# Kernel tuning notes

Measured on AMD Instinct MI355X. Metric: run time of the kernel, lower is better.

Reference implementation:

```python
import jax, jax.numpy as jnp
import numpy as np

IN_CH = 128
OUT_CH = 128
N_NODES = 50000
N_EDGES = 800000
BN_EPS = 1e-5


def setup_inputs() -> dict:
    key = jax.random.key(0)
    k_x, k_e, k_wl, k_bl, k_wr = jax.random.split(key, 5)
    x = jax.random.normal(k_x, (N_NODES, IN_CH), dtype=jnp.float32)
    edge_index = jax.random.randint(k_e, (2, N_EDGES), 0, N_NODES, dtype=jnp.int64)
    s = 1.0 / np.sqrt(IN_CH)
    W_l = jax.random.uniform(k_wl, (OUT_CH, IN_CH), jnp.float32, -s, s)  # lin_l: aggregated neighbors
    b_l = jax.random.uniform(k_bl, (OUT_CH,), jnp.float32, -s, s)
    W_r = jax.random.uniform(k_wr, (OUT_CH, IN_CH), jnp.float32, -s, s)  # lin_r: root/self
    gamma = jnp.ones((OUT_CH,), jnp.float32)
    beta = jnp.zeros((OUT_CH,), jnp.float32)
    return {"x": x, "edge_index": edge_index, "W_l": W_l, "b_l": b_l,
            "W_r": W_r, "gamma": gamma, "beta": beta}


def reference(x, edge_index, W_l, b_l, W_r, gamma, beta):
    n = x.shape[0]
    src, dst = edge_index[0], edge_index[1]
    # gather source features and mean-aggregate at destination nodes
    msgs = x[src]                                              # [E, C_in]
    agg = jax.ops.segment_sum(msgs, dst, num_segments=n)      # [N, C_in]
    deg = jax.ops.segment_sum(jnp.ones((edge_index.shape[1],), x.dtype), dst, num_segments=n)
    mean_agg = agg / jnp.maximum(deg, 1.0)[:, None]
    # SAGEConv: lin_l(aggregated) + lin_r(self)
    h = mean_agg @ W_l.T + b_l + x @ W_r.T                     # [N, C_out]
    # BatchNorm1d (training-mode batch statistics, biased variance)
    mu = h.mean(axis=0)
    var = ((h - mu) ** 2).mean(axis=0)
    h = (h - mu) * jax.lax.rsqrt(var + BN_EPS) * gamma + beta
    return jax.nn.relu(h)
```

## Files before the change

### kernel.cpp

```cpp
#include <hip/hip_runtime.h>

#define CH 128
#define BN_EPS 1e-5f

typedef unsigned int uint32;
typedef unsigned short ushort16;
using f32x2  = __attribute__((ext_vector_type(2))) float;
using f32x4  = __attribute__((ext_vector_type(4))) float;
using bf16x8 = __attribute__((ext_vector_type(8))) short;

__device__ __forceinline__ ushort16 f2b(float f) {
    uint32 u = __float_as_uint(f);
    return (ushort16)((u + 0x7FFFu + ((u >> 16) & 1u)) >> 16);
}
__device__ __forceinline__ uint32 pk2(float a, float b) {
    return (uint32)f2b(a) | ((uint32)f2b(b) << 16);
}
__device__ __forceinline__ float blo(uint32 u) { return __uint_as_float(u << 16); }
__device__ __forceinline__ float bhi(uint32 u) { return __uint_as_float(u & 0xFFFF0000u); }

__global__ __launch_bounds__(256) void sage_prep(
    const float* __restrict__ x, const void* __restrict__ ei,
    const float* __restrict__ Wl, const float* __restrict__ Wr,
    int* __restrict__ head, int2* __restrict__ pair,
    uint32* __restrict__ xb4, uint2* __restrict__ xq8,
    ushort16* __restrict__ wct, float* __restrict__ bn,
    int nEdges, int nNodes, int total8)
{
    const int* pi = (const int*)ei;
    int lane = threadIdx.x & 63;
    int probe = pi[lane * 2 + 1];
    bool is64 = (__ballot(probe != 0) == 0ULL);

    int idx = blockIdx.x * 256 + threadIdx.x;

    const float4* x4 = (const float4*)x;
    float4 a = make_float4(0, 0, 0, 0), b = make_float4(0, 0, 0, 0);
    bool hasC = (idx < total8);
    if (hasC) { a = x4[2 * idx]; b = x4[2 * idx + 1]; }

    if (idx < nEdges) {
        int s, d;
        if (is64) {
            const long long* p = (const long long*)ei;
            s = (int)p[idx];
            d = (int)p[nEdges + idx];
        } else {
            s = pi[idx];
            d = pi[nEdges + idx];
        }
        int old = atomicExch(&head[d], idx);
        pair[idx] = make_int2(old, s);
    }

    if (hasC) {
        uint4 o;
        o.x = pk2(a.x, a.y); o.y = pk2(a.z, a.w);
        o.z = pk2(b.x, b.y); o.w = pk2(b.z, b.w);
        ((uint4*)xb4)[idx] = o;

        int qa = __builtin_amdgcn_cvt_pk_fp8_f32(a.x, a.y, 0, false);
        qa = __builtin_amdgcn_cvt_pk_fp8_f32(a.z, a.w, qa, true);
        int qb = __builtin_amdgcn_cvt_pk_fp8_f32(b.x, b.y, 0, false);
        qb = __builtin_amdgcn_cvt_pk_fp8_f32(b.z, b.w, qb, true);
        xq8[idx] = make_uint2((uint32)qa, (uint32)qb);
    }

    if (blockIdx.x < 128) {
        int widx = blockIdx.x * 256 + threadIdx.x;
        int co = widx >> 8, k = widx & 255;
        float v = (k < 128) ? Wr[co * 128 + k] : Wl[co * 128 + (k - 128)];
        wct[widx] = f2b(v);
    }
    if (blockIdx.x == 0) bn[threadIdx.x] = 0.f;
    if (blockIdx.x == 1 && threadIdx.x < 32)
        ((uint32*)(xq8))[(size_t)total8 * 2 + threadIdx.x] = 0;
}

__global__ __launch_bounds__(256) void sage_init(int* __restrict__ head, int nNodes) {
    int i = blockIdx.x * 256 + threadIdx.x;
    if (i < nNodes) head[i] = -1;
}

__global__ __launch_bounds__(256) void sage_aggregate(
    const char* __restrict__ xq, const int* __restrict__ head,
    const int2* __restrict__ pair, uint32* __restrict__ mean_b, int nNodes)
{
    int wid = blockIdx.x * 4 + (threadIdx.x >> 6);
    int nbase = wid * 8;
    if (nbase >= nNodes) return;
    int lane = threadIdx.x & 63;
    int chain = lane >> 3;
    int sub = lane & 7;

    const int ZROW = nNodes;

    int cur = -1;
    if (lane < 8) {
        int n = nbase + lane;
        cur = (n < nNodes) ? head[n] : -1;
    }
    int cnt = 0;
    f32x2 acc2[8];
    #pragma unroll
    for (int i = 0; i < 8; ++i) acc2[i] = (f32x2){0.f, 0.f};

    int2 pr = make_int2(-1, ZROW);
    if (cur >= 0) pr = pair[cur];

    while (__ballot(cur >= 0) != 0ULL) {
        int nxt = pr.x;
        int2 prn = make_int2(-1, ZROW);
        if (cur >= 0 && nxt >= 0) prn = pair[nxt];

        int s = __shfl(pr.y, chain);
        uint4 u = *(const uint4*)(xq + ((size_t)s << 7) + sub * 16);
        #pragma unroll
        for (int w = 0; w < 4; ++w) {
            uint32 uw = (&u.x)[w];
            acc2[w * 2 + 0] += __builtin_amdgcn_cvt_pk_f32_fp8((int)uw, false);
            acc2[w * 2 + 1] += __builtin_amdgcn_cvt_pk_f32_fp8((int)uw, true);
        }
        if (cur >= 0) { ++cnt; cur = nxt; }
        pr = prn;
    }

    int cn = __shfl(cnt, chain);
    float inv = 1.0f / fmaxf((float)cn, 1.0f);
    int n = nbase + chain;
    if (n < nNodes) {
        uint4 o0 = make_uint4(pk2(acc2[0][0] * inv, acc2[0][1] * inv),
                              pk2(acc2[1][0] * inv, acc2[1][1] * inv),
                              pk2(acc2[2][0] * inv, acc2[2][1] * inv),
                              pk2(acc2[3][0] * inv, acc2[3][1] * inv));
        uint4 o1 = make_uint4(pk2(acc2[4][0] * inv, acc2[4][1] * inv),
                              pk2(acc2[5][0] * inv, acc2[5][1] * inv),
                              pk2(acc2[6][0] * inv, acc2[6][1] * inv),
                              pk2(acc2[7][0] * inv, acc2[7][1] * inv));
        char* base = (char*)mean_b + (size_t)n * 256 + sub * 32;
        *(uint4*)base = o0;
        *(uint4*)(base + 16) = o1;
    }
}

__global__ __launch_bounds__(256) void sage_gemm(
    const ushort16* __restrict__ xb, const ushort16* __restrict__ mean_b,
    const ushort16* __restrict__ wct, const float* __restrict__ bl,
    ushort16* __restrict__ hb, float* __restrict__ bn, int nNodes)
{
    __shared__ ushort16 wsh[8 * 8 * 64 * 8];
    __shared__ float redS[4][CH];
    __shared__ float redQ[4][CH];

    int tid = threadIdx.x;
    int wave = tid >> 6, lane = tid & 63;
    int col = lane & 15, kg = lane >> 4;

    #pragma unroll
    for (int it = 0; it < 16; ++it) {
        int pidx = wave * 16 + it;
        int cb = pidx >> 3, ks = pidx & 7;
        bf16x8 v = *(const bf16x8*)(wct + (size_t)(cb * 16 + col) * 256 + ks * 32 + kg * 8);
        *(bf16x8*)(wsh + ((size_t)pidx * 64 + lane) * 8) = v;
    }

    int row0 = blockIdx.x * 128 + wave * 16;
    int row1 = row0 + 64;
    int arow0 = min(row0 + col, nNodes - 1);
    int arow1 = min(row1 + col, nNodes - 1);
    const ushort16* xr0 = xb + (size_t)arow0 * CH;
    const ushort16* mr0 = mean_b + (size_t)arow0 * CH;
    const ushort16* xr1 = xb + (size_t)arow1 * CH;
    const ushort16* mr1 = mean_b + (size_t)arow1 * CH;

    bf16x8 af0[8], af1[8];
    #pragma unroll
    for (int t = 0; t < 4; ++t) {
        af0[t]     = *(const bf16x8*)(xr0 + t * 32 + kg * 8);
        af0[4 + t] = *(const bf16x8*)(mr0 + t * 32 + kg * 8);
        af1[t]     = *(const bf16x8*)(xr1 + t * 32 + kg * 8);
        af1[4 + t] = *(const bf16x8*)(mr1 + t * 32 + kg * 8);
    }

    __syncthreads();

    f32x4 acc0[8], acc1[8];
    #pragma unroll
    for (int cb = 0; cb < 8; ++cb) {
        acc0[cb] = (f32x4){0.f, 0.f, 0.f, 0.f};
        acc1[cb] = (f32x4){0.f, 0.f, 0.f, 0.f};
    }

    #pragma unroll
    for (int kstep = 0; kstep < 8; ++kstep) {
        #pragma unroll
        for (int cb = 0; cb < 8; ++cb) {
            bf16x8 b = *(const bf16x8*)(wsh + ((size_t)(cb * 8 + kstep) * 64 + lane) * 8);
            acc0[cb] = __builtin_amdgcn_mfma_f32_16x16x32_bf16(af0[kstep], b, acc0[cb], 0, 0, 0);
            acc1[cb] = __builtin_amdgcn_mfma_f32_16x16x32_bf16(af1[kstep], b, acc1[cb], 0, 0, 0);
        }
    }

    #pragma unroll
    for (int cb = 0; cb < 8; ++cb) {
        int co = cb * 16 + col;
        float blv = bl[co];
        float s = 0.f, ss = 0.f;
        #pragma unroll
        for (int j = 0; j < 4; ++j) {
            int r0 = row0 + kg * 4 + j;
            float v0 = acc0[cb][j] + blv;
            if (r0 < nNodes) {
                hb[(size_t)r0 * CH + co] = f2b(v0);
                s += v0; ss += v0 * v0;
            }
            int r1 = row1 + kg * 4 + j;
            float v1 = acc1[cb][j] + blv;
            if (r1 < nNodes) {
                hb[(size_t)r1 * CH + co] = f2b(v1);
                s += v1; ss += v1 * v1;
            }
        }
        s  += __shfl_xor(s, 16);  s  += __shfl_xor(s, 32);
        ss += __shfl_xor(ss, 16); ss += __shfl_xor(ss, 32);
        if (kg == 0) { redS[wave][co] = s; redQ[wave][co] = ss; }
    }
    __syncthreads();
    if (tid < CH) {
        atomicAdd(&bn[tid], redS[0][tid] + redS[1][tid] + redS[2][tid] + redS[3][tid]);
    } else {
        int c = tid - CH;
        atomicAdd(&bn[CH + c], redQ[0][c] + redQ[1][c] + redQ[2][c] + redQ[3][c]);
    }
}

__global__ __launch_bounds__(256) void sage_apply(
    const ushort16* __restrict__ hb, float* __restrict__ out,
    const float* __restrict__ bn, const float* __restrict__ gamma,
    const float* __restrict__ beta, int total8, int nNodes)
{
    __shared__ float sc_sh[CH], sh_sh[CH];
    int tid = threadIdx.x;
    if (tid < CH) {
        float invN = 1.0f / (float)nNodes;
        float mu = bn[tid] * invN;
        float var = fmaxf(bn[CH + tid] * invN - mu * mu, 0.f);
        float sc = gamma[tid] * rsqrtf(var + BN_EPS);
        sc_sh[tid] = sc;
        sh_sh[tid] = beta[tid] - mu * sc;
    }
    __syncthreads();
    int i = blockIdx.x * 256 + tid;
    if (i >= total8) return;
    uint4 u = *(const uint4*)(hb + (size_t)i * 8);
    int c = (i * 8) & 127;
    float4 o0, o1;
    o0.x = fmaxf(fmaf(blo(u.x), sc_sh[c + 0], sh_sh[c + 0]), 0.f);
    o0.y = fmaxf(fmaf(bhi(u.x), sc_sh[c + 1], sh_sh[c + 1]), 0.f);
    o0.z = fmaxf(fmaf(blo(u.y), sc_sh[c + 2], sh_sh[c + 2]), 0.f);
    o0.w = fmaxf(fmaf(bhi(u.y), sc_sh[c + 3], sh_sh[c + 3]), 0.f);
    o1.x = fmaxf(fmaf(blo(u.z), sc_sh[c + 4], sh_sh[c + 4]), 0.f);
    o1.y = fmaxf(fmaf(bhi(u.z), sc_sh[c + 5], sh_sh[c + 5]), 0.f);
    o1.z = fmaxf(fmaf(blo(u.w), sc_sh[c + 6], sh_sh[c + 6]), 0.f);
    o1.w = fmaxf(fmaf(bhi(u.w), sc_sh[c + 7], sh_sh[c + 7]), 0.f);
    float4* dst = (float4*)(out + (size_t)i * 8);
    dst[0] = o0;
    dst[1] = o1;
}

extern "C" void kernel_launch(void* const* d_in, const int* in_sizes, int n_in,
                              void* d_out, int out_size, void* d_ws, size_t ws_size,
                              hipStream_t stream)
{
    const float* x     = (const float*)d_in[0];
    const void*  ei    = d_in[1];
    const float* Wl    = (const float*)d_in[2];
    const float* bl    = (const float*)d_in[3];
    const float* Wr    = (const float*)d_in[4];
    const float* gamma = (const float*)d_in[5];
    const float* beta  = (const float*)d_in[6];

    int nNodes = in_sizes[0] / CH;
    int nEdges = in_sizes[1] / 2;
    int nBlkM  = (nNodes + 127) / 128;

    char* p = (char*)d_ws;
    auto take = [&](size_t bytes) {
        char* r = p;
        p += (bytes + 255) & ~(size_t)255;
        return r;
    };
    ushort16* xb      = (ushort16*)take((size_t)nNodes * CH * 2);
    char*     xq      = (char*)take((size_t)nNodes * CH + 128);
    ushort16* mean_b  = (ushort16*)take((size_t)nNodes * CH * 2);
    ushort16* hb      = (ushort16*)take((size_t)nNodes * CH * 2);
    ushort16* wct     = (ushort16*)take((size_t)CH * 256 * 2);
    int*      head    = (int*)take((size_t)nNodes * 4);
    float*    bn      = (float*)take(256 * 4);
    int2*     pair    = (int2*)take((size_t)nEdges * 8);

    float* out = (float*)d_out;

    int total8 = nNodes * CH / 8;
    int eBlocks = (nEdges + 255) / 256;
    int pBlocks = max(eBlocks, (total8 + 255) / 256);

    sage_init<<<(nNodes + 255) / 256, 256, 0, stream>>>(head, nNodes);

    sage_prep<<<pBlocks, 256, 0, stream>>>(
        x, ei, Wl, Wr, head, pair, (uint32*)xb, (uint2*)xq, wct, bn,
        nEdges, nNodes, total8);

    int aBlocks = (nNodes + 31) / 32;
    sage_aggregate<<<aBlocks, 256, 0, stream>>>(
        xq, head, pair, (uint32*)mean_b, nNodes);

    sage_gemm<<<nBlkM, 256, 0, stream>>>(
        xb, mean_b, wct, bl, hb, bn, nNodes);

    sage_apply<<<(total8 + 255) / 256, 256, 0, stream>>>(
        hb, out, bn, gamma, beta, total8, nNodes);
}
```

Measured before the change: 115.9 us.

## Overlap root GEMM with neighbor aggregation and split GEMM into two halves

The x@W_r^T half of the linear layer now runs inside the same launch as the neighbor aggregation, as extra blocks, and writes fp32 partial results in MFMA fragment layout. The second GEMM only multiplies the mean aggregate by W_l and accumulates onto those partials. Weight conversion and other init work move from the prep kernel into the init kernel, and prep loads are reordered to issue edge loads before the atomics. This hides the root GEMM behind the latency-bound gather, at the cost of an extra fp32 round trip through memory for the partial results.

```diff
diff --git a/kernel.cpp b/kernel.cpp
--- a/kernel.cpp
+++ b/kernel.cpp
@@ -19,28 +19,39 @@
 __device__ __forceinline__ float blo(uint32 u) { return __uint_as_float(u << 16); }
 __device__ __forceinline__ float bhi(uint32 u) { return __uint_as_float(u & 0xFFFF0000u); }
 
+__global__ __launch_bounds__(256) void sage_init(
+    const float* __restrict__ Wl, const float* __restrict__ Wr,
+    int* __restrict__ head, ushort16* __restrict__ wct,
+    float* __restrict__ bn, uint32* __restrict__ xqz, int nNodes)
+{
+    int i = blockIdx.x * 256 + threadIdx.x;
+    if (i < nNodes) head[i] = -1;
+    if (blockIdx.x < 128) {
+        int widx = blockIdx.x * 256 + threadIdx.x;
+        int co = widx >> 8, k = widx & 255;
+        float v = (k < 128) ? Wr[co * 128 + k] : Wl[co * 128 + (k - 128)];
+        wct[widx] = f2b(v);
+    }
+    if (blockIdx.x == 0) bn[threadIdx.x] = 0.f;
+    if (blockIdx.x == 1 && threadIdx.x < 32) xqz[threadIdx.x] = 0;
+}
+
 __global__ __launch_bounds__(256) void sage_prep(
     const float* __restrict__ x, const void* __restrict__ ei,
-    const float* __restrict__ Wl, const float* __restrict__ Wr,
     int* __restrict__ head, int2* __restrict__ pair,
     uint32* __restrict__ xb4, uint2* __restrict__ xq8,
-    ushort16* __restrict__ wct, float* __restrict__ bn,
-    int nEdges, int nNodes, int total8)
+    int nEdges, int total8)
 {
     const int* pi = (const int*)ei;
     int lane = threadIdx.x & 63;
-    int probe = pi[lane * 2 + 1];
-    bool is64 = (__ballot(probe != 0) == 0ULL);
+    bool is64 = (__ballot(pi[lane * 2 + 1] != 0) == 0ULL);
 
     int idx = blockIdx.x * 256 + threadIdx.x;
-
-    const float4* x4 = (const float4*)x;
-    float4 a = make_float4(0, 0, 0, 0), b = make_float4(0, 0, 0, 0);
+    bool hasE = (idx < nEdges);
     bool hasC = (idx < total8);
-    if (hasC) { a = x4[2 * idx]; b = x4[2 * idx + 1]; }
-
-    if (idx < nEdges) {
-        int s, d;
+
+    int s = 0, d = 0;
+    if (hasE) {
         if (is64) {
             const long long* p = (const long long*)ei;
             s = (int)p[idx];
@@ -49,9 +60,13 @@
             s = pi[idx];
             d = pi[nEdges + idx];
         }
-        int old = atomicExch(&head[d], idx);
-        pair[idx] = make_int2(old, s);
-    }
+    }
+    const float4* x4 = (const float4*)x;
+    float4 a = make_float4(0, 0, 0, 0), b = make_float4(0, 0, 0, 0);
+    if (hasC) { a = x4[2 * idx]; b = x4[2 * idx + 1]; }
+
+    int old = 0;
+    if (hasE) old = atomicExch(&head[d], idx);
 
     if (hasC) {
         uint4 o;
@@ -66,30 +81,70 @@
         xq8[idx] = make_uint2((uint32)qa, (uint32)qb);
     }
 
-    if (blockIdx.x < 128) {
-        int widx = blockIdx.x * 256 + threadIdx.x;
-        int co = widx >> 8, k = widx & 255;
-        float v = (k < 128) ? Wr[co * 128 + k] : Wl[co * 128 + (k - 128)];
-        wct[widx] = f2b(v);
-    }
-    if (blockIdx.x == 0) bn[threadIdx.x] = 0.f;
-    if (blockIdx.x == 1 && threadIdx.x < 32)
-        ((uint32*)(xq8))[(size_t)total8 * 2 + threadIdx.x] = 0;
-}
-
-__global__ __launch_bounds__(256) void sage_init(int* __restrict__ head, int nNodes) {
-    int i = blockIdx.x * 256 + threadIdx.x;
-    if (i < nNodes) head[i] = -1;
-}
-
-__global__ __launch_bounds__(256) void sage_aggregate(
+    if (hasE) pair[idx] = make_int2(old, s);
+}
+
+__global__ __launch_bounds__(256) void sage_mid(
+    const ushort16* __restrict__ xb, const ushort16* __restrict__ wct,
+    const float* __restrict__ bl, f32x4* __restrict__ h1f,
     const char* __restrict__ xq, const int* __restrict__ head,
-    const int2* __restrict__ pair, uint32* __restrict__ mean_b, int nNodes)
-{
-    int wid = blockIdx.x * 4 + (threadIdx.x >> 6);
+    const int2* __restrict__ pair, uint32* __restrict__ mean_b,
+    int g1, int nNodes)
+{
+    __shared__ ushort16 wsh[8 * 4 * 64 * 8];
+
+    int tid = threadIdx.x;
+    int wave = tid >> 6, lane = tid & 63;
+
+    if ((int)blockIdx.x < g1) {
+        int col = lane & 15, kg = lane >> 4;
+        #pragma unroll
+        for (int it = 0; it < 8; ++it) {
+            int pidx = wave * 8 + it;
+            int cb = pidx >> 2, ks = pidx & 3;
+            bf16x8 v = *(const bf16x8*)(wct + (size_t)(cb * 16 + col) * 256 + ks * 32 + kg * 8);
+            *(bf16x8*)(wsh + ((size_t)pidx * 64 + lane) * 8) = v;
+        }
+
+        int gid = blockIdx.x;
+        int rowBase = gid * 64 + wave * 16;
+        int arow = min(rowBase + col, nNodes - 1);
+        const ushort16* xrow = xb + (size_t)arow * CH;
+
+        bf16x8 af[4];
+        #pragma unroll
+        for (int t = 0; t < 4; ++t)
+            af[t] = *(const bf16x8*)(xrow + t * 32 + kg * 8);
+
+        __syncthreads();
+
+        f32x4 acc[8];
+        #pragma unroll
+        for (int cb = 0; cb < 8; ++cb) acc[cb] = (f32x4){0.f, 0.f, 0.f, 0.f};
+
+        #pragma unroll
+        for (int ks = 0; ks < 4; ++ks) {
+            #pragma unroll
+            for (int cb = 0; cb < 8; ++cb) {
+                bf16x8 b = *(const bf16x8*)(wsh + ((size_t)(cb * 4 + ks) * 64 + lane) * 8);
+                acc[cb] = __builtin_amdgcn_mfma_f32_16x16x32_bf16(af[ks], b, acc[cb], 0, 0, 0);
+            }
+        }
+
+        #pragma unroll
+        for (int cb = 0; cb < 8; ++cb) {
+            float blv = bl[cb * 16 + col];
+            f32x4 v = acc[cb];
+            v[0] += blv; v[1] += blv; v[2] += blv; v[3] += blv;
+            h1f[(((size_t)gid * 4 + wave) * 8 + cb) * 64 + lane] = v;
+        }
+        return;
+    }
+
+    int aid = blockIdx.x - g1;
+    int wid = aid * 4 + wave;
     int nbase = wid * 8;
     if (nbase >= nNodes) return;
-    int lane = threadIdx.x & 63;
     int chain = lane >> 3;
     int sub = lane & 7;
 
@@ -143,12 +198,12 @@
     }
 }
 
-__global__ __launch_bounds__(256) void sage_gemm(
-    const ushort16* __restrict__ xb, const ushort16* __restrict__ mean_b,
-    const ushort16* __restrict__ wct, const float* __restrict__ bl,
-    ushort16* __restrict__ hb, float* __restrict__ bn, int nNodes)
-{
-    __shared__ ushort16 wsh[8 * 8 * 64 * 8];
+__global__ __launch_bounds__(256) void sage_gemm2(
+    const ushort16* __restrict__ mean_b, const ushort16* __restrict__ wct,
+    const f32x4* __restrict__ h1f, ushort16* __restrict__ hb,
+    float* __restrict__ bn, int nNodes)
+{
+    __shared__ ushort16 wsh[8 * 4 * 64 * 8];
     __shared__ float redS[4][CH];
     __shared__ float redQ[4][CH];
 
@@ -157,65 +212,61 @@
     int col = lane & 15, kg = lane >> 4;
 
     #pragma unroll
-    for (int it = 0; it < 16; ++it) {
-        int pidx = wave * 16 + it;
-        int cb = pidx >> 3, ks = pidx & 7;
-        bf16x8 v = *(const bf16x8*)(wct + (size_t)(cb * 16 + col) * 256 + ks * 32 + kg * 8);
+    for (int it = 0; it < 8; ++it) {
+        int pidx = wave * 8 + it;
+        int cb = pidx >> 2, ks = pidx & 3;
+        bf16x8 v = *(const bf16x8*)(wct + (size_t)(cb * 16 + col) * 256 + 128 + ks * 32 + kg * 8);
         *(bf16x8*)(wsh + ((size_t)pidx * 64 + lane) * 8) = v;
     }
 
-    int row0 = blockIdx.x * 128 + wave * 16;
-    int row1 = row0 + 64;
+    int gid0 = blockIdx.x * 2, gid1 = gid0 + 1;
+    int row0 = gid0 * 64 + wave * 16;
+    int row1 = gid1 * 64 + wave * 16;
     int arow0 = min(row0 + col, nNodes - 1);
     int arow1 = min(row1 + col, nNodes - 1);
-    const ushort16* xr0 = xb + (size_t)arow0 * CH;
     const ushort16* mr0 = mean_b + (size_t)arow0 * CH;
-    const ushort16* xr1 = xb + (size_t)arow1 * CH;
     const ushort16* mr1 = mean_b + (size_t)arow1 * CH;
 
-    bf16x8 af0[8], af1[8];
+    bf16x8 af0[4], af1[4];
     #pragma unroll
     for (int t = 0; t < 4; ++t) {
-        af0[t]     = *(const bf16x8*)(xr0 + t * 32 + kg * 8);
-        af0[4 + t] = *(const bf16x8*)(mr0 + t * 32 + kg * 8);
-        af1[t]     = *(const bf16x8*)(xr1 + t * 32 + kg * 8);
-        af1[4 + t] = *(const bf16x8*)(mr1 + t * 32 + kg * 8);
+        af0[t] = *(const bf16x8*)(mr0 + t * 32 + kg * 8);
+        af1[t] = *(const bf16x8*)(mr1 + t * 32 + kg * 8);
+    }
+
+    f32x4 acc0[8], acc1[8];
+    #pragma unroll
+    for (int cb = 0; cb < 8; ++cb) {
+        acc0[cb] = h1f[(((size_t)gid0 * 4 + wave) * 8 + cb) * 64 + lane];
+        acc1[cb] = h1f[(((size_t)gid1 * 4 + wave) * 8 + cb) * 64 + lane];
     }
 
     __syncthreads();
 
-    f32x4 acc0[8], acc1[8];
-    #pragma unroll
-    for (int cb = 0; cb < 8; ++cb) {
-        acc0[cb] = (f32x4){0.f, 0.f, 0.f, 0.f};
-        acc1[cb] = (f32x4){0.f, 0.f, 0.f, 0.f};
-    }
-
-    #pragma unroll
-    for (int kstep = 0; kstep < 8; ++kstep) {
+    #pragma unroll
+    for (int ks = 0; ks < 4; ++ks) {
         #pragma unroll
         for (int cb = 0; cb < 8; ++cb) {
-            bf16x8 b = *(const bf16x8*)(wsh + ((size_t)(cb * 8 + kstep) * 64 + lane) * 8);
-            acc0[cb] = __builtin_amdgcn_mfma_f32_16x16x32_bf16(af0[kstep], b, acc0[cb], 0, 0, 0);
-            acc1[cb] = __builtin_amdgcn_mfma_f32_16x16x32_bf16(af1[kstep], b, acc1[cb], 0, 0, 0);
+            bf16x8 b = *(const bf16x8*)(wsh + ((size_t)(cb * 4 + ks) * 64 + lane) * 8);
+            acc0[cb] = __builtin_amdgcn_mfma_f32_16x16x32_bf16(af0[ks], b, acc0[cb], 0, 0, 0);
+            acc1[cb] = __builtin_amdgcn_mfma_f32_16x16x32_bf16(af1[ks], b, acc1[cb], 0, 0, 0);
         }
     }
 
     #pragma unroll
     for (int cb = 0; cb < 8; ++cb) {
         int co = cb * 16 + col;
-        float blv = bl[co];
         float s = 0.f, ss = 0.f;
         #pragma unroll
         for (int j = 0; j < 4; ++j) {
             int r0 = row0 + kg * 4 + j;
-            float v0 = acc0[cb][j] + blv;
+            float v0 = acc0[cb][j];
             if (r0 < nNodes) {
                 hb[(size_t)r0 * CH + co] = f2b(v0);
                 s += v0; ss += v0 * v0;
             }
             int r1 = row1 + kg * 4 + j;
-            float v1 = acc1[cb][j] + blv;
+            float v1 = acc1[cb][j];
             if (r1 < nNodes) {
                 hb[(size_t)r1 * CH + co] = f2b(v1);
                 s += v1; ss += v1 * v1;
@@ -282,7 +333,9 @@
 
     int nNodes = in_sizes[0] / CH;
     int nEdges = in_sizes[1] / 2;
-    int nBlkM  = (nNodes + 127) / 128;
+    int g1     = (nNodes + 63) / 64;
+    int g2     = (nNodes + 127) / 128;
+    int aBlk   = (nNodes + 31) / 32;
 
     char* p = (char*)d_ws;
     auto take = [&](size_t bytes) {
@@ -294,6 +347,7 @@
     char*     xq      = (char*)take((size_t)nNodes * CH + 128);
     ushort16* mean_b  = (ushort16*)take((size_t)nNodes * CH * 2);
     ushort16* hb      = (ushort16*)take((size_t)nNodes * CH * 2);
+    f32x4*    h1f     = (f32x4*)take((size_t)g1 * 4 * 8 * 64 * 16);
     ushort16* wct     = (ushort16*)take((size_t)CH * 256 * 2);
     int*      head    = (int*)take((size_t)nNodes * 4);
     float*    bn      = (float*)take(256 * 4);
@@ -304,19 +358,19 @@
     int total8 = nNodes * CH / 8;
     int eBlocks = (nEdges + 255) / 256;
     int pBlocks = max(eBlocks, (total8 + 255) / 256);
-
-    sage_init<<<(nNodes + 255) / 256, 256, 0, stream>>>(head, nNodes);
+    int iBlocks = max((nNodes + 255) / 256, 128);
+
+    sage_init<<<iBlocks, 256, 0, stream>>>(
+        Wl, Wr, head, wct, bn, (uint32*)(xq + (size_t)nNodes * CH), nNodes);
 
     sage_prep<<<pBlocks, 256, 0, stream>>>(
-        x, ei, Wl, Wr, head, pair, (uint32*)xb, (uint2*)xq, wct, bn,
-        nEdges, nNodes, total8);
-
-    int aBlocks = (nNodes + 31) / 32;
-    sage_aggregate<<<aBlocks, 256, 0, stream>>>(
-        xq, head, pair, (uint32*)mean_b, nNodes);
-
-    sage_gemm<<<nBlkM, 256, 0, stream>>>(
-        xb, mean_b, wct, bl, hb, bn, nNodes);
+        x, ei, head, pair, (uint32*)xb, (uint2*)xq, nEdges, total8);
+
+    sage_mid<<<g1 + aBlk, 256, 0, stream>>>(
+        xb, wct, bl, h1f, xq, head, pair, (uint32*)mean_b, g1, nNodes);
+
+    sage_gemm2<<<g2, 256, 0, stream>>>(
+        mean_b, wct, h1f, hb, bn, nNodes);
 
     sage_apply<<<(total8 + 255) / 256, 256, 0, stream>>>(
         hb, out, bn, gamma, beta, total8, nNodes);
```

Result: slower. 129.3 us (+11.6%).
